# Kernel optimization log

Measured on AMD Instinct MI355X. Metric: run time of the kernel, lower is better.

The kernel has to match this reference:

```python
import jax, jax.numpy as jnp
import numpy as np

N_HEAD = 16


def setup_inputs() -> dict:
    key = jax.random.key(0)
    k1, k2, k3 = jax.random.split(key, 3)
    B, T, N = 4, 2048, 1024
    x = jax.random.normal(k1, (B, T, N), dtype=jnp.float32)
    W_attn = jax.random.normal(k2, (N, 3 * N), dtype=jnp.float32) * (1.0 / np.sqrt(N))
    b_attn = jnp.zeros((3 * N,), dtype=jnp.float32)
    W_proj = jax.random.normal(k3, (N, N), dtype=jnp.float32) * (1.0 / np.sqrt(N))
    b_proj = jnp.zeros((N,), dtype=jnp.float32)
    return {"x": x, "W_attn": W_attn, "b_attn": b_attn, "W_proj": W_proj, "b_proj": b_proj}


def reference(x, W_attn, b_attn, W_proj, b_proj):
    B, T, N = x.shape
    H = N_HEAD
    Dh = N // H
    qkv = x @ W_attn + b_attn                      # [B, T, 3N]
    q, k, v = jnp.split(qkv, 3, axis=2)
    # [B, H, T, Dh]
    q = q.reshape(B, T, H, Dh).transpose(0, 2, 1, 3)
    k = k.reshape(B, T, H, Dh).transpose(0, 2, 1, 3)
    v = v.reshape(B, T, H, Dh).transpose(0, 2, 1, 3)
    att = jnp.einsum('bhqd,bhkd->bhqk', q, k) / (Dh ** 0.5)
    mask = jnp.tril(jnp.ones((T, T), dtype=bool))
    att = jnp.where(mask[None, None], att, jnp.finfo(x.dtype).min)
    att = jax.nn.softmax(att, axis=-1)
    y = jnp.einsum('bhqk,bhkd->bhqd', att, v)      # [B, H, T, Dh]
    y = y.transpose(0, 2, 1, 3).reshape(B, T, N)
    return y @ W_proj + b_proj
```

## Files before the change

kernel.cpp:

```cpp
#include <hip/hip_runtime.h>
#include <hip/hip_bf16.h>


typedef __attribute__((ext_vector_type(8))) short short8;
typedef __attribute__((ext_vector_type(4))) float f32x4;
typedef __attribute__((ext_vector_type(16))) float f32x16;

#define MFMA16(a, b, c) __builtin_amdgcn_mfma_f32_16x16x32_bf16((a), (b), (c), 0, 0, 0)
#define MFMA32(a, b, c) __builtin_amdgcn_mfma_f32_32x32x16_bf16((a), (b), (c), 0, 0, 0)

#if defined(__has_builtin)
#if __has_builtin(__builtin_amdgcn_exp2f)
#define EXP2(x) __builtin_amdgcn_exp2f(x)
#endif
#endif
#ifndef EXP2
#define EXP2(x) exp2f(x)
#endif

__device__ __forceinline__ void gload_lds16(const void* g, void* l) {
  __builtin_amdgcn_global_load_lds(
      (const __attribute__((address_space(1))) unsigned int*)g,
      (__attribute__((address_space(3))) unsigned int*)l, 16, 0, 0);
}

__device__ __forceinline__ unsigned pack_bf16x2(float lo, float hi) {
  unsigned ulo = __float_as_uint(lo) + 0x8000u;
  unsigned uhi = __float_as_uint(hi) + 0x8000u;
  return __builtin_amdgcn_perm(uhi, ulo, 0x07060302u);
}

__device__ __forceinline__ unsigned short bf16u(float f) {
  return (unsigned short)((__float_as_uint(f) + 0x8000u) >> 16);
}

__global__ void conv_f32_bf16(const float* __restrict__ src,
                              unsigned* __restrict__ dst, int n4) {
  int i = blockIdx.x * blockDim.x + threadIdx.x;
  if (i >= n4) return;
  float4 v = ((const float4*)src)[i];
  uint2 o;
  o.x = pack_bf16x2(v.x, v.y);
  o.y = pack_bf16x2(v.z, v.w);
  ((uint2*)dst)[i] = o;
}

__global__ void transpose_bf16(const float* __restrict__ src,
                               __hip_bfloat16* __restrict__ dst, int R, int C) {
  __shared__ float tile[32][33];
  int tx = threadIdx.x, ty = threadIdx.y;
  int c0 = blockIdx.x * 32, r0 = blockIdx.y * 32;
#pragma unroll
  for (int i = 0; i < 32; i += 8)
    tile[ty + i][tx] = src[(long)(r0 + ty + i) * C + c0 + tx];
  __syncthreads();
#pragma unroll
  for (int i = 0; i < 32; i += 8)
    dst[(long)(c0 + ty + i) * R + r0 + tx] = __float2bfloat16(tile[tx][ty + i]);
}

template <int EPI>
__global__ __launch_bounds__(256, 2) void gemm_bt(
    const __hip_bfloat16* __restrict__ A, const __hip_bfloat16* __restrict__ Bt,
    const float* __restrict__ bias, void* o0, void* o1, void* o2, int N, int K) {
  __shared__ alignas(16) char smem[34816];
  short8 (*As)[8] = (short8(*)[8])smem;
  short8 (*Bs)[8] = (short8(*)[8])(smem + 16384);
  unsigned short (*C16)[136] = (unsigned short(*)[136])smem;
  float (*C32)[132] = (float(*)[132])smem;

  const int tid = threadIdx.x;
  const int lane = tid & 63, w = tid >> 6;
  const int l15 = lane & 15, quad = lane >> 4;
  const int wm = (w >> 1) * 64, wn = (w & 1) * 64;
  const int rowBase = blockIdx.y * 128;
  const int colBase = blockIdx.x * 128;
  const int sr8 = lane >> 3;
  const int scc = (lane & 7) ^ sr8;

  f32x4 acc[4][4];
#pragma unroll
  for (int mi = 0; mi < 4; ++mi)
#pragma unroll
    for (int ni = 0; ni < 4; ++ni)
      acc[mi][ni] = {0.f, 0.f, 0.f, 0.f};

  for (int k0 = 0; k0 < K; k0 += 64) {
    __syncthreads();
#pragma unroll
    for (int p = 0; p < 4; ++p) {
      const int rb = p * 32 + w * 8;
      const int row = rb + sr8;
      gload_lds16(A + (rowBase + row) * K + k0 + scc * 8, &As[rb][0]);
      gload_lds16(Bt + (colBase + row) * K + k0 + scc * 8, &Bs[rb][0]);
    }
    __syncthreads();
#pragma unroll
    for (int kc = 0; kc < 2; ++kc) {
      short8 af[4], bf[4];
#pragma unroll
      for (int mi = 0; mi < 4; ++mi) {
        int row = wm + mi * 16 + l15;
        af[mi] = As[row][(kc * 4 + quad) ^ (row & 7)];
      }
#pragma unroll
      for (int ni = 0; ni < 4; ++ni) {
        int row = wn + ni * 16 + l15;
        bf[ni] = Bs[row][(kc * 4 + quad) ^ (row & 7)];
      }
#pragma unroll
      for (int mi = 0; mi < 4; ++mi)
#pragma unroll
        for (int ni = 0; ni < 4; ++ni)
          acc[mi][ni] = MFMA16(af[mi], bf[ni], acc[mi][ni]);
    }
  }

  float bcol[4];
#pragma unroll
  for (int ni = 0; ni < 4; ++ni) bcol[ni] = bias[colBase + wn + ni * 16 + l15];

  if (EPI == 0) {
    const int which = colBase >> 10;
    const int b = rowBase >> 11;
    const int tt0 = rowBase & 2047;
    const int n1base = colBase & 1023;
    const float osc = (which == 0) ? 0.180336880111f : 1.0f;
    __syncthreads();
    if (which != 2) {
#pragma unroll
      for (int mi = 0; mi < 4; ++mi)
#pragma unroll
        for (int ni = 0; ni < 4; ++ni)
#pragma unroll
          for (int r = 0; r < 4; ++r)
            C16[wm + mi * 16 + quad * 4 + r][wn + ni * 16 + l15] =
                bf16u((acc[mi][ni][r] + bcol[ni]) * osc);
    } else {
#pragma unroll
      for (int mi = 0; mi < 4; ++mi)
#pragma unroll
        for (int ni = 0; ni < 4; ++ni)
#pragma unroll
          for (int r = 0; r < 4; ++r)
            C16[wn + ni * 16 + l15][wm + mi * 16 + quad * 4 + r] =
                bf16u(acc[mi][ni][r] + bcol[ni]);
    }
    __syncthreads();
    unsigned short* o = (unsigned short*)(which == 0 ? o0 : which == 1 ? o1 : o2);
    if (which != 2) {
#pragma unroll
      for (int j = 0; j < 8; ++j) {
        int flat = j * 256 + tid;
        int trow = flat >> 4, ch = flat & 15;
        int h = (n1base + ((ch & 8) << 3)) >> 6;
        long addr = ((long)((b * 16 + h) * 2048 + tt0 + trow)) * 64 + (ch & 7) * 8;
        *(short8*)&o[addr] = *(const short8*)&C16[trow][ch * 8];
      }
    } else {
#pragma unroll
      for (int j = 0; j < 8; ++j) {
        int flat = j * 256 + tid;
        int dcol = flat >> 4, ch = flat & 15;
        int h = (n1base + (dcol & 64)) >> 6;
        long addr = ((long)((b * 16 + h) * 64 + (dcol & 63))) * 2048 + tt0 + ch * 8;
        *(short8*)&o[addr] = *(const short8*)&C16[dcol][ch * 8];
      }
    }
  } else {
    float* out = (float*)o0;
    for (int p = 0; p < 2; ++p) {
      __syncthreads();
      if ((w >> 1) == p) {
#pragma unroll
        for (int mi = 0; mi < 4; ++mi)
#pragma unroll
          for (int ni = 0; ni < 4; ++ni)
#pragma unroll
            for (int r = 0; r < 4; ++r)
              C32[mi * 16 + quad * 4 + r][wn + ni * 16 + l15] =
                  acc[mi][ni][r] + bcol[ni];
      }
      __syncthreads();
#pragma unroll
      for (int j = 0; j < 8; ++j) {
        int flat = j * 256 + tid;
        int row = flat >> 5, ch = flat & 31;
        float4 v4 = *(const float4*)&C32[row][ch * 4];
        *(float4*)&out[(long)(rowBase + p * 64 + row) * N + colBase + ch * 4] = v4;
      }
    }
  }
}

__global__ __launch_bounds__(256, 4) void attn_kernel(
    const __hip_bfloat16* __restrict__ Q, const __hip_bfloat16* __restrict__ K,
    const __hip_bfloat16* __restrict__ Vt, __hip_bfloat16* __restrict__ Y, int T) {
  __shared__ short8 Ks[2][64][8];
  __shared__ short8 Vs[2][64][8];
  const int tid = threadIdx.x;
  const int w = tid >> 6, lane = tid & 63;
  const int c31 = lane & 31, half = lane >> 5;
  const int rsw = c31 & 7;
  const int idx = blockIdx.x;
  const int bh = idx & 63;
  const int b = bh >> 4, h = bh & 15;
  const int qsel = idx >> 6;
  const int qq = qsel >> 2, qp = qsel & 3;
  const int jt = (qq == 0) ? 15 - qp : (qq == 1) ? 8 + qp : (qq == 2) ? 4 + qp : 3 - qp;

  const int qrow0 = jt * 128 + w * 32;
  const __hip_bfloat16* Qp = Q + (long)bh * T * 64;
  const __hip_bfloat16* Kp = K + (long)bh * T * 64;
  const __hip_bfloat16* Vp = Vt + (long)bh * 64 * T;

  const int sr8 = lane >> 3;
  const int scc = (lane & 7) ^ sr8;

  short8 qf[4];
#pragma unroll
  for (int s = 0; s < 4; ++s)
    qf[s] = *(const short8*)(Qp + (qrow0 + c31) * 64 + s * 16 + half * 8);

  f32x16 czero;
#pragma unroll
  for (int i = 0; i < 16; ++i) czero[i] = 0.f;
  f32x16 oacc[2];
#pragma unroll
  for (int g = 0; g < 2; ++g) oacc[g] = czero;
  float lsum = 0.f;
  const int myq = qrow0 + c31;
  const int nkt = 2 * jt + 2;
  const int my_nkt = 2 * jt + 1 + (w >> 1);
  const int my_diag = my_nkt - 1;

#define STAGE_ATTN(buf, kbase)                                                 \
  do {                                                                         \
    const int rb_ = w * 16;                                                    \
    gload_lds16(Kp + ((kbase) + rb_ + sr8) * 64 + scc * 8, &Ks[buf][rb_][0]);  \
    gload_lds16(Kp + ((kbase) + rb_ + 8 + sr8) * 64 + scc * 8,                 \
                &Ks[buf][rb_ + 8][0]);                                         \
    gload_lds16(Vp + (long)(rb_ + sr8) * T + (kbase) + scc * 8,                \
                &Vs[buf][rb_][0]);                                             \
    gload_lds16(Vp + (long)(rb_ + 8 + sr8) * T + (kbase) + scc * 8,            \
                &Vs[buf][rb_ + 8][0]);                                         \
  } while (0)

  STAGE_ATTN(0, 0);
  __syncthreads();

  for (int kt = 0; kt < nkt; ++kt) {
    const int bb = kt & 1;
    const int kb = kt * 64;
    if (kt + 1 < nkt) STAGE_ATTN(bb ^ 1, kb + 64);

    if (kt < my_nkt) {
      short8 pb[4];
#pragma unroll
      for (int g = 0; g < 2; ++g) {
        f32x16 z = MFMA32(Ks[bb][g * 32 + c31][half ^ rsw], qf[0], czero);
#pragma unroll
        for (int s = 1; s < 4; ++s) {
          short8 af = Ks[bb][g * 32 + c31][(s * 2 + half) ^ rsw];
          z = MFMA32(af, qf[s], z);
        }
        if (kt == my_diag) {
#pragma unroll
          for (int r = 0; r < 16; ++r) {
            int key = kb + g * 32 + (r & 3) + 8 * (r >> 2) + 4 * half;
            if (key > myq) z[r] = -INFINITY;
          }
        }
        unsigned pk[8];
#pragma unroll
        for (int i = 0; i < 8; ++i) {
          float p0 = EXP2(z[2 * i]);
          float p1 = EXP2(z[2 * i + 1]);
          lsum += p0 + p1;
          pk[i] = pack_bf16x2(p0, p1);
        }
#pragma unroll
        for (int s = 0; s < 2; ++s) {
          auto r0 = __builtin_amdgcn_permlane32_swap(pk[4 * s + 0], pk[4 * s + 2],
                                                     false, false);
          auto r1 = __builtin_amdgcn_permlane32_swap(pk[4 * s + 1], pk[4 * s + 3],
                                                     false, false);
          union { unsigned u[4]; short8 s8; } cv;
          cv.u[0] = r0[0]; cv.u[1] = r1[0]; cv.u[2] = r0[1]; cv.u[3] = r1[1];
          pb[g * 2 + s] = cv.s8;
        }
      }
#pragma unroll
      for (int dg = 0; dg < 2; ++dg)
#pragma unroll
        for (int S = 0; S < 4; ++S) {
          short8 vf = Vs[bb][dg * 32 + c31][(S * 2 + half) ^ rsw];
          oacc[dg] = MFMA32(vf, pb[S], oacc[dg]);
        }
    }
    __syncthreads();
  }

  lsum += __shfl_xor(lsum, 32);

  const float inv = 1.0f / lsum;
  unsigned short* Yu = (unsigned short*)Y;
  const long rowoff = ((long)(b * 2048 + qrow0 + c31)) * 1024 + h * 64;
#pragma unroll
  for (int dg = 0; dg < 2; ++dg)
#pragma unroll
    for (int rg = 0; rg < 4; ++rg) {
      uint2 o;
      o.x = pack_bf16x2(oacc[dg][rg * 4 + 0] * inv, oacc[dg][rg * 4 + 1] * inv);
      o.y = pack_bf16x2(oacc[dg][rg * 4 + 2] * inv, oacc[dg][rg * 4 + 3] * inv);
      *(uint2*)&Yu[rowoff + dg * 32 + half * 4 + rg * 8] = o;
    }
}

extern "C" void kernel_launch(void* const* d_in, const int* in_sizes, int n_in,
                              void* d_out, int out_size, void* d_ws, size_t ws_size,
                              hipStream_t stream) {
  const float* x  = (const float*)d_in[0];
  const float* Wa = (const float*)d_in[1];
  const float* ba = (const float*)d_in[2];
  const float* Wp = (const float*)d_in[3];
  const float* bp = (const float*)d_in[4];
  float* out = (float*)d_out;

  char* ws = (char*)d_ws;
  __hip_bfloat16* Xb  = (__hip_bfloat16*)(ws);
  __hip_bfloat16* WaT = (__hip_bfloat16*)(ws + 16777216);
  __hip_bfloat16* WpT = (__hip_bfloat16*)(ws + 23068672);
  __hip_bfloat16* Qb  = (__hip_bfloat16*)(ws + 25165824);
  __hip_bfloat16* Kb  = (__hip_bfloat16*)(ws + 41943040);
  __hip_bfloat16* Vtb = (__hip_bfloat16*)(ws + 58720256);
  __hip_bfloat16* Yb  = (__hip_bfloat16*)(ws + 75497472);
  if (ws_size < 92274688) return;

  conv_f32_bf16<<<8192, 256, 0, stream>>>(x, (unsigned*)Xb, 2097152);
  transpose_bf16<<<dim3(96, 32), dim3(32, 8), 0, stream>>>(Wa, WaT, 1024, 3072);
  transpose_bf16<<<dim3(32, 32), dim3(32, 8), 0, stream>>>(Wp, WpT, 1024, 1024);
  gemm_bt<0><<<dim3(24, 64), 256, 0, stream>>>(Xb, WaT, ba, Qb, Kb, Vtb, 3072, 1024);
  attn_kernel<<<dim3(1024), dim3(256), 0, stream>>>(Qb, Kb, Vtb, Yb, 2048);
  gemm_bt<1><<<dim3(8, 64), 256, 0, stream>>>(Yb, WpT, bp, out, nullptr, nullptr, 1024, 1024);
}
```

Before: 230.8 us.

## Triple-buffer attention K/V loads and fuse prep kernels into one launch

The attention kernel moves from double to triple buffering of K/V tiles in LDS. Loads are issued two tiles ahead, and one s_waitcnt plus barrier per iteration replaces the two __syncthreads, so more memory latency can overlap compute. Launch bounds drop from 4 to 3 blocks per CU to fit the extra LDS. Separately, the x conversion and the two weight transposes are merged into a single prep kernel to save launch overhead. The lower occupancy may cancel part of the latency-hiding gain.

```diff
diff --git a/kernel.cpp b/kernel.cpp
--- a/kernel.cpp
+++ b/kernel.cpp
@@ -34,22 +34,32 @@
   return (unsigned short)((__float_as_uint(f) + 0x8000u) >> 16);
 }
 
-__global__ void conv_f32_bf16(const float* __restrict__ src,
-                              unsigned* __restrict__ dst, int n4) {
-  int i = blockIdx.x * blockDim.x + threadIdx.x;
-  if (i >= n4) return;
-  float4 v = ((const float4*)src)[i];
-  uint2 o;
-  o.x = pack_bf16x2(v.x, v.y);
-  o.y = pack_bf16x2(v.z, v.w);
-  ((uint2*)dst)[i] = o;
-}
-
-__global__ void transpose_bf16(const float* __restrict__ src,
-                               __hip_bfloat16* __restrict__ dst, int R, int C) {
+__global__ void prep_kernel(const float* __restrict__ x, unsigned* __restrict__ Xb,
+                            const float* __restrict__ Wa, __hip_bfloat16* __restrict__ WaT,
+                            const float* __restrict__ Wp, __hip_bfloat16* __restrict__ WpT) {
   __shared__ float tile[32][33];
-  int tx = threadIdx.x, ty = threadIdx.y;
-  int c0 = blockIdx.x * 32, r0 = blockIdx.y * 32;
+  const int tid = threadIdx.x;
+  int blk = blockIdx.x;
+  if (blk >= 4096) {
+    int i = (blk - 4096) * 256 + tid;
+    float4 v = ((const float4*)x)[i];
+    uint2 o;
+    o.x = pack_bf16x2(v.x, v.y);
+    o.y = pack_bf16x2(v.z, v.w);
+    ((uint2*)Xb)[i] = o;
+    return;
+  }
+  const float* src;
+  __hip_bfloat16* dst;
+  int R, C, bx, by;
+  if (blk < 3072) {
+    src = Wa; dst = WaT; R = 1024; C = 3072; bx = blk % 96; by = blk / 96;
+  } else {
+    blk -= 3072;
+    src = Wp; dst = WpT; R = 1024; C = 1024; bx = blk & 31; by = blk >> 5;
+  }
+  const int tx = tid & 31, ty = tid >> 5;
+  const int c0 = bx * 32, r0 = by * 32;
 #pragma unroll
   for (int i = 0; i < 32; i += 8)
     tile[ty + i][tx] = src[(long)(r0 + ty + i) * C + c0 + tx];
@@ -193,11 +203,11 @@
   }
 }
 
-__global__ __launch_bounds__(256, 4) void attn_kernel(
+__global__ __launch_bounds__(256, 3) void attn_kernel(
     const __hip_bfloat16* __restrict__ Q, const __hip_bfloat16* __restrict__ K,
     const __hip_bfloat16* __restrict__ Vt, __hip_bfloat16* __restrict__ Y, int T) {
-  __shared__ short8 Ks[2][64][8];
-  __shared__ short8 Vs[2][64][8];
+  __shared__ short8 Ks[3][64][8];
+  __shared__ short8 Vs[3][64][8];
   const int tid = threadIdx.x;
   const int w = tid >> 6, lane = tid & 63;
   const int c31 = lane & 31, half = lane >> 5;
@@ -247,21 +257,31 @@
   } while (0)
 
   STAGE_ATTN(0, 0);
-  __syncthreads();
+  STAGE_ATTN(1, 64);
+  int bcur = 0;
 
   for (int kt = 0; kt < nkt; ++kt) {
-    const int bb = kt & 1;
-    const int kb = kt * 64;
-    if (kt + 1 < nkt) STAGE_ATTN(bb ^ 1, kb + 64);
+    if (kt < nkt - 1)
+      asm volatile("s_waitcnt vmcnt(4)" ::: "memory");
+    else
+      asm volatile("s_waitcnt vmcnt(0)" ::: "memory");
+    __builtin_amdgcn_s_barrier();
+    __builtin_amdgcn_sched_barrier(0);
+
+    if (kt + 2 < nkt) {
+      const int bs = (bcur >= 1) ? bcur - 1 : 2;
+      STAGE_ATTN(bs, (kt + 2) * 64);
+    }
 
     if (kt < my_nkt) {
+      const int kb = kt * 64;
       short8 pb[4];
 #pragma unroll
       for (int g = 0; g < 2; ++g) {
-        f32x16 z = MFMA32(Ks[bb][g * 32 + c31][half ^ rsw], qf[0], czero);
+        f32x16 z = MFMA32(Ks[bcur][g * 32 + c31][half ^ rsw], qf[0], czero);
 #pragma unroll
         for (int s = 1; s < 4; ++s) {
-          short8 af = Ks[bb][g * 32 + c31][(s * 2 + half) ^ rsw];
+          short8 af = Ks[bcur][g * 32 + c31][(s * 2 + half) ^ rsw];
           z = MFMA32(af, qf[s], z);
         }
         if (kt == my_diag) {
@@ -294,11 +314,11 @@
       for (int dg = 0; dg < 2; ++dg)
 #pragma unroll
         for (int S = 0; S < 4; ++S) {
-          short8 vf = Vs[bb][dg * 32 + c31][(S * 2 + half) ^ rsw];
+          short8 vf = Vs[bcur][dg * 32 + c31][(S * 2 + half) ^ rsw];
           oacc[dg] = MFMA32(vf, pb[S], oacc[dg]);
         }
     }
-    __syncthreads();
+    bcur = (bcur == 2) ? 0 : bcur + 1;
   }
 
   lsum += __shfl_xor(lsum, 32);
@@ -337,9 +357,7 @@
   __hip_bfloat16* Yb  = (__hip_bfloat16*)(ws + 75497472);
   if (ws_size < 92274688) return;
 
-  conv_f32_bf16<<<8192, 256, 0, stream>>>(x, (unsigned*)Xb, 2097152);
-  transpose_bf16<<<dim3(96, 32), dim3(32, 8), 0, stream>>>(Wa, WaT, 1024, 3072);
-  transpose_bf16<<<dim3(32, 32), dim3(32, 8), 0, stream>>>(Wp, WpT, 1024, 1024);
+  prep_kernel<<<12288, 256, 0, stream>>>(x, (unsigned*)Xb, Wa, WaT, Wp, WpT);
   gemm_bt<0><<<dim3(24, 64), 256, 0, stream>>>(Xb, WaT, ba, Qb, Kb, Vtb, 3072, 1024);
   attn_kernel<<<dim3(1024), dim3(256), 0, stream>>>(Qb, Kb, Vtb, Yb, 2048);
   gemm_bt<1><<<dim3(8, 64), 256, 0, stream>>>(Yb, WpT, bp, out, nullptr, nullptr, 1024, 1024);
```

Result: faster. 222.7 us (-3.5%).
